# Kernel tuning notes

Hardware: AMD Instinct MI355X
Metric: run time of the kernel (lower is better)

## Reference

```python
import jax, jax.numpy as jnp
import numpy as np

N_EMBD = 512
N_HEAD = 8
HEAD = N_EMBD // N_HEAD
EPS = 1e-5

def layernorm(x, g, b):
    mu = jnp.mean(x, axis=-1, keepdims=True)
    var = jnp.mean(jnp.square(x - mu), axis=-1, keepdims=True)
    return (x - mu) * jax.lax.rsqrt(var + EPS) * g + b

def setup_inputs() -> dict:
    key = jax.random.key(0)
    ks = jax.random.split(key, 12)
    B, T, C, H, D = 32, 512, N_EMBD, N_HEAD, HEAD
    s = lambda fan: 1.0 / np.sqrt(fan)
    return {
        "x": jax.random.normal(ks[0], (B, T, C), jnp.float32),
        "wq": jax.random.normal(ks[1], (H, C, D), jnp.float32) * s(C),
        "wk": jax.random.normal(ks[2], (H, C, D), jnp.float32) * s(C),
        "wv": jax.random.normal(ks[3], (H, C, D), jnp.float32) * s(C),
        "w_proj": jax.random.normal(ks[4], (C, C), jnp.float32) * s(C),
        "b_proj": jnp.zeros((C,), jnp.float32),
        "w1": jax.random.normal(ks[5], (C, 4 * C), jnp.float32) * s(C),
        "b1": jnp.zeros((4 * C,), jnp.float32),
        "w2": jax.random.normal(ks[6], (4 * C, C), jnp.float32) * s(4 * C),
        "b2": jnp.zeros((C,), jnp.float32),
        "ln1_g": jnp.ones((C,), jnp.float32),
        "ln1_b": jnp.zeros((C,), jnp.float32),
        "ln2_g": jnp.ones((C,), jnp.float32),
        "ln2_b": jnp.zeros((C,), jnp.float32),
    }

def reference(x, wq, wk, wv, w_proj, b_proj, w1, b1, w2, b2, ln1_g, ln1_b, ln2_g, ln2_b):
    B, T, C = x.shape
    h = layernorm(x, ln1_g, ln1_b)
    q = jnp.einsum('btc,hcd->bhtd', h, wq)
    k = jnp.einsum('btc,hcd->bhtd', h, wk)
    v = jnp.einsum('btc,hcd->bhtd', h, wv)
    # NB: original scales by n_embd**-0.5 (C), not head_size
    scores = jnp.einsum('bhtd,bhsd->bhts', q, k) * (C ** -0.5)
    causal = jnp.tril(jnp.ones((T, T), bool))
    scores = jnp.where(causal, scores, -jnp.inf)
    attn = jax.nn.softmax(scores, axis=-1)
    o = jnp.einsum('bhts,bhsd->bhtd', attn, v)  # [B,H,T,D]
    o = jnp.transpose(o, (0, 2, 1, 3)).reshape(B, T, C)  # concat heads
    x = x + o @ w_proj + b_proj
    h2 = layernorm(x, ln2_g, ln2_b)
    ffn = jax.nn.relu(h2 @ w1 + b1) @ w2 + b2
    return x + ffn
```

## Files before the change

kernel.cpp:

```cpp
#include <hip/hip_runtime.h>
#include <hip/hip_bf16.h>


#define B_  32
#define T_  512
#define C_  512
#define H_  8
#define D_  64
#define BT  (B_*T_)
#define CF  2048

typedef __hip_bfloat16 bf16;
typedef __attribute__((ext_vector_type(8))) short bf16x8;
typedef __attribute__((ext_vector_type(4))) float f32x4;
typedef __attribute__((ext_vector_type(4))) short short4v;

__device__ __forceinline__ float bf2f(bf16 x) { return __bfloat162float(x); }
__device__ __forceinline__ bf16  f2bf(float x){ return __float2bfloat16(x); }
__device__ __forceinline__ short f2bf_bits(float f){
    bf16 h = __float2bfloat16(f);
    return *reinterpret_cast<short*>(&h);
}
__device__ __forceinline__ float bfbits2f(short s){
    unsigned u = ((unsigned)(unsigned short)s) << 16;
    return __uint_as_float(u);
}

#define AS_G __attribute__((address_space(1)))
#define AS_L __attribute__((address_space(3)))

__global__ __launch_bounds__(256) void transpose_all(const float* __restrict__ wq,
                                                     const float* __restrict__ wk,
                                                     const float* __restrict__ wv,
                                                     const float* __restrict__ wproj,
                                                     const float* __restrict__ w1,
                                                     const float* __restrict__ w2,
                                                     bf16* __restrict__ wt)
{
    const int t = blockIdx.x;
    const float* src; int K, Nn, k0, n0; size_t dstoff;
    if (t < 192) {
        const int which = t / 64, w = t % 64, hh = w >> 3, kt = w & 7;
        src = (which == 0 ? wq : which == 1 ? wk : wv) + (size_t)hh * 512 * 64;
        K = 512; Nn = 64; k0 = kt * 64; n0 = 0;
        dstoff = (size_t)(which * 512 + hh * 64) * 512;
    } else if (t < 256) {
        const int i = t - 192;
        src = wproj; K = 512; Nn = 512; n0 = (i & 7) * 64; k0 = (i >> 3) * 64;
        dstoff = (size_t)1536 * 512;
    } else if (t < 512) {
        const int i = t - 256;
        src = w1; K = 512; Nn = 2048; n0 = (i & 31) * 64; k0 = (i >> 5) * 64;
        dstoff = (size_t)2048 * 512;
    } else {
        const int i = t - 512;
        src = w2; K = 2048; Nn = 512; n0 = (i & 7) * 64; k0 = (i >> 3) * 64;
        dstoff = (size_t)2048 * 512 + (size_t)2048 * 512;
    }

    __shared__ float tl[64][65];
    const int tid = threadIdx.x;
    #pragma unroll
    for (int j = 0; j < 16; ++j) {
        const int e = j * 256 + tid, r = e >> 6, c = e & 63;
        tl[r][c] = src[(size_t)(k0 + r) * Nn + n0 + c];
    }
    __syncthreads();
    #pragma unroll
    for (int j = 0; j < 16; ++j) {
        const int e = j * 256 + tid, n = e >> 6, kk = e & 63;
        wt[dstoff + (size_t)(n0 + n) * K + k0 + kk] = f2bf(tl[kk][n]);
    }
}

__global__ __launch_bounds__(256) void ln_kernel(const float* __restrict__ x,
                                                 const float* __restrict__ g,
                                                 const float* __restrict__ b,
                                                 bf16* __restrict__ out)
{
    const int row = blockIdx.x;
    const int tid = threadIdx.x;
    const float* xr = x + (size_t)row * C_;
    float v0 = xr[tid], v1 = xr[tid + 256];

    __shared__ float red[4];

    float s = v0 + v1;
    #pragma unroll
    for (int off = 32; off > 0; off >>= 1) s += __shfl_down(s, off, 64);
    if ((tid & 63) == 0) red[tid >> 6] = s;
    __syncthreads();
    const float mean = (red[0] + red[1] + red[2] + red[3]) * (1.0f / C_);
    __syncthreads();

    float d0 = v0 - mean, d1 = v1 - mean;
    float vs = d0 * d0 + d1 * d1;
    #pragma unroll
    for (int off = 32; off > 0; off >>= 1) vs += __shfl_down(vs, off, 64);
    if ((tid & 63) == 0) red[tid >> 6] = vs;
    __syncthreads();
    const float var  = (red[0] + red[1] + red[2] + red[3]) * (1.0f / C_);
    const float rstd = rsqrtf(var + 1e-5f);

    bf16* orow = out + (size_t)row * C_;
    orow[tid]       = f2bf(d0 * rstd * g[tid]       + b[tid]);
    orow[tid + 256] = f2bf(d1 * rstd * g[tid + 256] + b[tid + 256]);
}

template<bool QKV, bool RELU, bool OUT_BF16>
__global__ __launch_bounds__(256, 2) void mfma_gemm(const bf16* __restrict__ A,
                                                    const bf16* __restrict__ Bt,
                                                    const float* __restrict__ bias,
                                                    const float* __restrict__ res,
                                                    void* __restrict__ outp,
                                                    int N, int K)
{
    __shared__ __align__(16) bf16 As[2][128 * 64];
    __shared__ __align__(16) bf16 Bs[2][128 * 64];

    const int tid  = threadIdx.x;
    const int wave = tid >> 6, lane = tid & 63;
    const int l16  = lane & 15, quad = lane >> 4;
    const int wm   = wave >> 1, wn = wave & 1;

    const int nwg = gridDim.x * gridDim.y;
    int bid = blockIdx.y * gridDim.x + blockIdx.x;
    bid = (bid & 7) * (nwg >> 3) + (bid >> 3);
    const int tn = (bid % gridDim.x) * 128;
    const int tm = (bid / gridDim.x) * 128;
    const bool vblk = QKV && (tn >= 1024);

    f32x4 acc[4][4];
    #pragma unroll
    for (int i = 0; i < 4; ++i)
        #pragma unroll
        for (int j = 0; j < 4; ++j) acc[i][j] = (f32x4){0.f, 0.f, 0.f, 0.f};

    auto STAGE = [&](int buf, int k0) {
        #pragma unroll
        for (int j = 0; j < 4; ++j) {
            const int g = j * 256 + tid;
            const int row = g >> 3, phys = g & 7;
            const int c = phys ^ (row & 7);
            __builtin_amdgcn_global_load_lds((const AS_G void*)(A  + (size_t)(tm + row) * K + k0 + c * 8),
                                             (AS_L void*)&As[buf][(size_t)g * 8], 16, 0, 0);
            __builtin_amdgcn_global_load_lds((const AS_G void*)(Bt + (size_t)(tn + row) * K + k0 + c * 8),
                                             (AS_L void*)&Bs[buf][(size_t)g * 8], 16, 0, 0);
        }
    };

    STAGE(0, 0);
    __syncthreads();

    int cur = 0;
    for (int k0 = 0; k0 < K; k0 += 64) {
        if (k0 + 64 < K) STAGE(cur ^ 1, k0 + 64);

        #pragma unroll
        for (int half = 0; half < 2; ++half) {
            bf16x8 af[4], bfr[4];
            #pragma unroll
            for (int mf = 0; mf < 4; ++mf) {
                const int r = wm * 64 + mf * 16 + l16;
                const int p = (half * 4 + quad) ^ (r & 7);
                af[mf] = *(const bf16x8*)&As[cur][r * 64 + p * 8];
            }
            #pragma unroll
            for (int nf = 0; nf < 4; ++nf) {
                const int r = wn * 64 + nf * 16 + l16;
                const int p = (half * 4 + quad) ^ (r & 7);
                bfr[nf] = *(const bf16x8*)&Bs[cur][r * 64 + p * 8];
            }
            if (vblk) {
                #pragma unroll
                for (int mf = 0; mf < 4; ++mf)
                    #pragma unroll
                    for (int nf = 0; nf < 4; ++nf)
                        acc[mf][nf] = __builtin_amdgcn_mfma_f32_16x16x32_bf16(af[mf], bfr[nf], acc[mf][nf], 0, 0, 0);
            } else {
                #pragma unroll
                for (int mf = 0; mf < 4; ++mf)
                    #pragma unroll
                    for (int nf = 0; nf < 4; ++nf)
                        acc[mf][nf] = __builtin_amdgcn_mfma_f32_16x16x32_bf16(bfr[nf], af[mf], acc[mf][nf], 0, 0, 0);
            }
        }

        __syncthreads();
        cur ^= 1;
    }

    if (QKV) {
        bf16* qkv = (bf16*)outp;
        if (!vblk) {
            const int which = tn >> 9;
            bf16* dst = qkv + (size_t)which * (8u << 20);
            #pragma unroll
            for (int mf = 0; mf < 4; ++mf) {
                const int m = tm + wm * 64 + mf * 16 + l16;
                const int bb = m >> 9, t = m & 511;
                #pragma unroll
                for (int nf = 0; nf < 4; ++nf) {
                    const int nb = tn + wn * 64 + nf * 16 + quad * 4;
                    const int hh = (nb >> 6) & 7, dd = nb & 63;
                    short4v pk;
                    #pragma unroll
                    for (int r = 0; r < 4; ++r) pk[r] = f2bf_bits(acc[mf][nf][r]);
                    *(short4v*)&dst[((size_t)(bb * 8 + hh) * 512 + t) * 64 + dd] = pk;
                }
            }
        } else {
            bf16* dst = qkv + (size_t)2 * (8u << 20);
            #pragma unroll
            for (int mf = 0; mf < 4; ++mf) {
                const int mb = tm + wm * 64 + mf * 16 + quad * 4;
                const int bb = mb >> 9, t = mb & 511;
                #pragma unroll
                for (int nf = 0; nf < 4; ++nf) {
                    const int n = tn + wn * 64 + nf * 16 + l16;
                    const int hh = (n >> 6) & 7, dd = n & 63;
                    short4v pk;
                    #pragma unroll
                    for (int r = 0; r < 4; ++r) pk[r] = f2bf_bits(acc[mf][nf][r]);
                    *(short4v*)&dst[((size_t)(bb * 8 + hh) * 64 + dd) * 512 + t] = pk;
                }
            }
        }
    } else {
        #pragma unroll
        for (int mf = 0; mf < 4; ++mf) {
            const int m = tm + wm * 64 + mf * 16 + l16;
            #pragma unroll
            for (int nf = 0; nf < 4; ++nf) {
                const int nb = tn + wn * 64 + nf * 16 + quad * 4;
                f32x4 a = acc[mf][nf];
                if (bias) a += *(const f32x4*)&bias[nb];
                if (RELU) {
                    #pragma unroll
                    for (int r = 0; r < 4; ++r) a[r] = fmaxf(a[r], 0.0f);
                }
                if (res)  a += *(const f32x4*)&res[(size_t)m * N + nb];
                if (OUT_BF16) {
                    short4v pk;
                    #pragma unroll
                    for (int r = 0; r < 4; ++r) pk[r] = f2bf_bits(a[r]);
                    *(short4v*)&((bf16*)outp)[(size_t)m * N + nb] = pk;
                } else {
                    *(f32x4*)&((float*)outp)[(size_t)m * N + nb] = a;
                }
            }
        }
    }
}

__global__ __launch_bounds__(256) void attn_kernel(const bf16* __restrict__ q,
                                                   const bf16* __restrict__ kM,
                                                   const bf16* __restrict__ vT,
                                                   bf16* __restrict__ o)
{
    __shared__ __align__(16) bf16 Ks[64][72];
    __shared__ __align__(16) bf16 Vt[64][72];
    __shared__ __align__(16) bf16 Pw[4][16][72];

    const int qt   = gridDim.x - 1 - blockIdx.x;
    const int bh   = blockIdx.y;
    const int tid  = threadIdx.x;
    const int wave = tid >> 6, lane = tid & 63;
    const int l16  = lane & 15, quad = lane >> 4;
    const int qw   = qt * 64 + wave * 16;

    const float scale = 0.04419417382415922f;
    bf16x8 qa[2];
    #pragma unroll
    for (int c = 0; c < 2; ++c) {
        const bf16* qp = q + ((size_t)bh * T_ + qw + l16) * 64 + c * 32 + quad * 8;
        bf16x8 t = *(const bf16x8*)qp;
        #pragma unroll
        for (int j = 0; j < 8; ++j) t[j] = f2bf_bits(bfbits2f(t[j]) * scale);
        qa[c] = t;
    }

    float m_i[4], l_i[4];
    f32x4 Of[4];
    #pragma unroll
    for (int r = 0; r < 4; ++r) { m_i[r] = -1e30f; l_i[r] = 0.0f; }
    #pragma unroll
    for (int f = 0; f < 4; ++f) Of[f] = (f32x4){0.f, 0.f, 0.f, 0.f};

    for (int kt = 0; kt <= qt; ++kt) {
        const int k0 = kt * 64;
        __syncthreads();
        #pragma unroll
        for (int c2 = 0; c2 < 2; ++c2) {
            const int ch = tid + c2 * 256;
            const int row = ch >> 3, e8 = (ch & 7) * 8;
            *(uint4*)&Ks[row][e8] = *(const uint4*)(kM + ((size_t)bh * T_ + k0 + row) * 64 + e8);
            *(uint4*)&Vt[row][e8] = *(const uint4*)(vT + ((size_t)bh * 64 + row) * T_ + k0 + e8);
        }
        __syncthreads();

        f32x4 Sf[4];
        #pragma unroll
        for (int kf = 0; kf < 4; ++kf) {
            bf16x8 b0 = *(const bf16x8*)&Ks[kf * 16 + l16][quad * 8];
            bf16x8 b1 = *(const bf16x8*)&Ks[kf * 16 + l16][32 + quad * 8];
            f32x4 z = (f32x4){0.f, 0.f, 0.f, 0.f};
            z = __builtin_amdgcn_mfma_f32_16x16x32_bf16(qa[0], b0, z, 0, 0, 0);
            z = __builtin_amdgcn_mfma_f32_16x16x32_bf16(qa[1], b1, z, 0, 0, 0);
            Sf[kf] = z;
        }

        if (kt == qt) {
            #pragma unroll
            for (int kf = 0; kf < 4; ++kf)
                #pragma unroll
                for (int r = 0; r < 4; ++r)
                    if (k0 + kf * 16 + l16 > qw + quad * 4 + r) Sf[kf][r] = -1e30f;
        }

        float mnew[4], alpha[4];
        #pragma unroll
        for (int r = 0; r < 4; ++r) {
            float v = fmaxf(fmaxf(Sf[0][r], Sf[1][r]), fmaxf(Sf[2][r], Sf[3][r]));
            v = fmaxf(v, __shfl_xor(v, 1, 64));
            v = fmaxf(v, __shfl_xor(v, 2, 64));
            v = fmaxf(v, __shfl_xor(v, 4, 64));
            v = fmaxf(v, __shfl_xor(v, 8, 64));
            mnew[r]  = fmaxf(m_i[r], v);
            alpha[r] = __expf(m_i[r] - mnew[r]);
            m_i[r]   = mnew[r];
        }

        float rs[4] = {0.f, 0.f, 0.f, 0.f};
        #pragma unroll
        for (int kf = 0; kf < 4; ++kf) {
            #pragma unroll
            for (int r = 0; r < 4; ++r) {
                float p = __expf(Sf[kf][r] - mnew[r]);
                rs[r] += p;
                Pw[wave][quad * 4 + r][kf * 16 + l16] = f2bf(p);
            }
        }
        #pragma unroll
        for (int r = 0; r < 4; ++r) {
            rs[r] += __shfl_xor(rs[r], 1, 64);
            rs[r] += __shfl_xor(rs[r], 2, 64);
            rs[r] += __shfl_xor(rs[r], 4, 64);
            rs[r] += __shfl_xor(rs[r], 8, 64);
            l_i[r] = l_i[r] * alpha[r] + rs[r];
        }
        #pragma unroll
        for (int f = 0; f < 4; ++f)
            #pragma unroll
            for (int r = 0; r < 4; ++r)
                Of[f][r] *= alpha[r];

        bf16x8 pa0 = *(const bf16x8*)&Pw[wave][l16][quad * 8];
        bf16x8 pa1 = *(const bf16x8*)&Pw[wave][l16][32 + quad * 8];
        #pragma unroll
        for (int f = 0; f < 4; ++f) {
            bf16x8 vb0 = *(const bf16x8*)&Vt[f * 16 + l16][quad * 8];
            bf16x8 vb1 = *(const bf16x8*)&Vt[f * 16 + l16][32 + quad * 8];
            Of[f] = __builtin_amdgcn_mfma_f32_16x16x32_bf16(pa0, vb0, Of[f], 0, 0, 0);
            Of[f] = __builtin_amdgcn_mfma_f32_16x16x32_bf16(pa1, vb1, Of[f], 0, 0, 0);
        }
    }

    const int b = bh >> 3, hh = bh & 7;
    #pragma unroll
    for (int r = 0; r < 4; ++r) {
        const float inv = 1.0f / l_i[r];
        const int t = qw + quad * 4 + r;
        #pragma unroll
        for (int f = 0; f < 4; ++f)
            o[((size_t)b * T_ + t) * C_ + hh * 64 + f * 16 + l16] = f2bf(Of[f][r] * inv);
    }
}

extern "C" void kernel_launch(void* const* d_in, const int* in_sizes, int n_in,
                              void* d_out, int out_size, void* d_ws, size_t ws_size,
                              hipStream_t stream)
{
    const float* x     = (const float*)d_in[0];
    const float* wq    = (const float*)d_in[1];
    const float* wk    = (const float*)d_in[2];
    const float* wv    = (const float*)d_in[3];
    const float* wproj = (const float*)d_in[4];
    const float* bproj = (const float*)d_in[5];
    const float* w1    = (const float*)d_in[6];
    const float* b1    = (const float*)d_in[7];
    const float* w2    = (const float*)d_in[8];
    const float* b2    = (const float*)d_in[9];
    const float* ln1g  = (const float*)d_in[10];
    const float* ln1b  = (const float*)d_in[11];
    const float* ln2g  = (const float*)d_in[12];
    const float* ln2b  = (const float*)d_in[13];

    char* ws = (char*)d_ws;
    bf16*  h    = (bf16*)(ws + 0);
    bf16*  q    = (bf16*)(ws + ((size_t)16 << 20));
    bf16*  k    = (bf16*)(ws + ((size_t)32 << 20));
    bf16*  v    = (bf16*)(ws + ((size_t)48 << 20));
    bf16*  mid  = (bf16*)(ws + 0);
    bf16*  o    = (bf16*)(ws + ((size_t)64 << 20));
    bf16*  h2   = (bf16*)(ws + ((size_t)80 << 20));
    bf16*  wt   = (bf16*)(ws + ((size_t)96 << 20));
    bf16*  projt = wt + (size_t)1536 * 512;
    bf16*  w1t   = wt + (size_t)2048 * 512;
    bf16*  w2t   = wt + (size_t)4096 * 512;
    float* x1    = (float*)d_out;

    transpose_all<<<768, 256, 0, stream>>>(wq, wk, wv, wproj, w1, w2, wt);

    ln_kernel<<<BT, 256, 0, stream>>>(x, ln1g, ln1b, h);

    mfma_gemm<true,  false, true ><<<dim3(12, 128), 256, 0, stream>>>(h, wt, nullptr, nullptr, q, 1536, 512);

    attn_kernel<<<dim3(8, B_ * H_), 256, 0, stream>>>(q, k, v, o);

    mfma_gemm<false, false, false><<<dim3(4, 128), 256, 0, stream>>>(o, projt, bproj, x, x1, 512, 512);

    ln_kernel<<<BT, 256, 0, stream>>>(x1, ln2g, ln2b, h2);

    mfma_gemm<false, true,  true ><<<dim3(16, 128), 256, 0, stream>>>(h2, w1t, b1, nullptr, mid, 2048, 512);

    mfma_gemm<false, false, false><<<dim3(4, 128), 256, 0, stream>>>(mid, w2t, b2, x1, (float*)d_out, 512, 2048);
}
```

Measured before the change: 356.6 us.

## Pair causal query tiles per block with double-buffered async K/V staging

Each attention workgroup now handles two query tiles (qt and 7-qt), so every block does the same amount of causal work and shares each staged K/V tile between both. K/V tiles go through global_load_lds into swizzled double buffers, so the next tile loads while the current one is computed, and one barrier per iteration replaces two. Block IDs are remapped for locality, launch bounds request 2 blocks per SM, and the grid is halved. The cost is higher register pressure from two sets of accumulators, and the code depends on AS_G/AS_L macros that are defined elsewhere in the file.

```diff
diff --git a/kernel.cpp b/kernel.cpp
--- a/kernel.cpp
+++ b/kernel.cpp
@@ -253,127 +253,158 @@
     }
 }
 
-__global__ __launch_bounds__(256) void attn_kernel(const bf16* __restrict__ q,
-                                                   const bf16* __restrict__ kM,
-                                                   const bf16* __restrict__ vT,
-                                                   bf16* __restrict__ o)
+
+#define ATTN_TILE(qa, m_i, l_i, Of, qw, qtT)                                          \
+  do {                                                                                \
+    f32x4 Sf[4];                                                                      \
+    _Pragma("unroll")                                                                 \
+    for (int kf = 0; kf < 4; ++kf) {                                                  \
+        const int row = kf * 16 + l16;                                                \
+        bf16x8 b0 = *(const bf16x8*)&Ks[cur][row * 64 + ((quad ^ (row & 7)) * 8)];    \
+        bf16x8 b1 = *(const bf16x8*)&Ks[cur][row * 64 + (((4 + quad) ^ (row & 7)) * 8)]; \
+        f32x4 z = (f32x4){0.f, 0.f, 0.f, 0.f};                                        \
+        z = __builtin_amdgcn_mfma_f32_16x16x32_bf16(qa[0], b0, z, 0, 0, 0);           \
+        z = __builtin_amdgcn_mfma_f32_16x16x32_bf16(qa[1], b1, z, 0, 0, 0);           \
+        Sf[kf] = z;                                                                   \
+    }                                                                                 \
+    if (kt == qtT) {                                                                  \
+        _Pragma("unroll")                                                             \
+        for (int kf = 0; kf < 4; ++kf)                                                \
+            _Pragma("unroll")                                                         \
+            for (int r = 0; r < 4; ++r)                                               \
+                if (kt * 64 + kf * 16 + l16 > (qw) + quad * 4 + r) Sf[kf][r] = -1e30f;\
+    }                                                                                 \
+    float mnew[4], alpha[4];                                                          \
+    _Pragma("unroll")                                                                 \
+    for (int r = 0; r < 4; ++r) {                                                     \
+        float v = fmaxf(fmaxf(Sf[0][r], Sf[1][r]), fmaxf(Sf[2][r], Sf[3][r]));        \
+        v = fmaxf(v, __shfl_xor(v, 1, 64));                                           \
+        v = fmaxf(v, __shfl_xor(v, 2, 64));                                           \
+        v = fmaxf(v, __shfl_xor(v, 4, 64));                                           \
+        v = fmaxf(v, __shfl_xor(v, 8, 64));                                           \
+        mnew[r]   = fmaxf(m_i[r], v);                                                 \
+        alpha[r]  = __expf(m_i[r] - mnew[r]);                                         \
+        m_i[r]    = mnew[r];                                                          \
+    }                                                                                 \
+    float rs[4] = {0.f, 0.f, 0.f, 0.f};                                               \
+    _Pragma("unroll")                                                                 \
+    for (int kf = 0; kf < 4; ++kf) {                                                  \
+        _Pragma("unroll")                                                             \
+        for (int r = 0; r < 4; ++r) {                                                 \
+            float p = __expf(Sf[kf][r] - mnew[r]);                                    \
+            rs[r] += p;                                                               \
+            Pw[wave][quad * 4 + r][kf * 16 + l16] = f2bf(p);                          \
+        }                                                                             \
+    }                                                                                 \
+    _Pragma("unroll")                                                                 \
+    for (int r = 0; r < 4; ++r) {                                                     \
+        rs[r] += __shfl_xor(rs[r], 1, 64);                                            \
+        rs[r] += __shfl_xor(rs[r], 2, 64);                                            \
+        rs[r] += __shfl_xor(rs[r], 4, 64);                                            \
+        rs[r] += __shfl_xor(rs[r], 8, 64);                                            \
+        l_i[r] = l_i[r] * alpha[r] + rs[r];                                           \
+    }                                                                                 \
+    _Pragma("unroll")                                                                 \
+    for (int f = 0; f < 4; ++f)                                                       \
+        _Pragma("unroll")                                                             \
+        for (int r = 0; r < 4; ++r)                                                   \
+            Of[f][r] *= alpha[r];                                                     \
+    bf16x8 pa0 = *(const bf16x8*)&Pw[wave][l16][quad * 8];                            \
+    bf16x8 pa1 = *(const bf16x8*)&Pw[wave][l16][32 + quad * 8];                       \
+    _Pragma("unroll")                                                                 \
+    for (int f = 0; f < 4; ++f) {                                                     \
+        const int vrow = f * 16 + l16;                                                \
+        bf16x8 vb0 = *(const bf16x8*)&Vt[cur][vrow * 64 + ((quad ^ (vrow & 7)) * 8)]; \
+        bf16x8 vb1 = *(const bf16x8*)&Vt[cur][vrow * 64 + (((4 + quad) ^ (vrow & 7)) * 8)]; \
+        Of[f] = __builtin_amdgcn_mfma_f32_16x16x32_bf16(pa0, vb0, Of[f], 0, 0, 0);    \
+        Of[f] = __builtin_amdgcn_mfma_f32_16x16x32_bf16(pa1, vb1, Of[f], 0, 0, 0);    \
+    }                                                                                 \
+  } while (0)
+
+__global__ __launch_bounds__(256, 2) void attn_kernel(const bf16* __restrict__ q,
+                                                      const bf16* __restrict__ kM,
+                                                      const bf16* __restrict__ vT,
+                                                      bf16* __restrict__ o)
 {
-    __shared__ __align__(16) bf16 Ks[64][72];
-    __shared__ __align__(16) bf16 Vt[64][72];
+    __shared__ __align__(16) bf16 Ks[2][64 * 64];
+    __shared__ __align__(16) bf16 Vt[2][64 * 64];
     __shared__ __align__(16) bf16 Pw[4][16][72];
 
-    const int qt   = gridDim.x - 1 - blockIdx.x;
-    const int bh   = blockIdx.y;
     const int tid  = threadIdx.x;
     const int wave = tid >> 6, lane = tid & 63;
     const int l16  = lane & 15, quad = lane >> 4;
-    const int qw   = qt * 64 + wave * 16;
+
+    const int nwg = gridDim.x * gridDim.y;
+    int bid = blockIdx.y * gridDim.x + blockIdx.x;
+    bid = (bid & 7) * (nwg >> 3) + (bid >> 3);
+    const int pair = bid & 3;
+    const int bh   = bid >> 2;
+
+    const int qt0 = pair, qt1 = 7 - pair;
+    const int qw0 = qt0 * 64 + wave * 16;
+    const int qw1 = qt1 * 64 + wave * 16;
 
     const float scale = 0.04419417382415922f;
-    bf16x8 qa[2];
+    bf16x8 qa0[2], qa1[2];
     #pragma unroll
     for (int c = 0; c < 2; ++c) {
-        const bf16* qp = q + ((size_t)bh * T_ + qw + l16) * 64 + c * 32 + quad * 8;
-        bf16x8 t = *(const bf16x8*)qp;
-        #pragma unroll
-        for (int j = 0; j < 8; ++j) t[j] = f2bf_bits(bfbits2f(t[j]) * scale);
-        qa[c] = t;
-    }
-
-    float m_i[4], l_i[4];
-    f32x4 Of[4];
-    #pragma unroll
-    for (int r = 0; r < 4; ++r) { m_i[r] = -1e30f; l_i[r] = 0.0f; }
-    #pragma unroll
-    for (int f = 0; f < 4; ++f) Of[f] = (f32x4){0.f, 0.f, 0.f, 0.f};
-
-    for (int kt = 0; kt <= qt; ++kt) {
+        bf16x8 t0 = *(const bf16x8*)(q + ((size_t)bh * T_ + qw0 + l16) * 64 + c * 32 + quad * 8);
+        bf16x8 t1 = *(const bf16x8*)(q + ((size_t)bh * T_ + qw1 + l16) * 64 + c * 32 + quad * 8);
+        #pragma unroll
+        for (int j = 0; j < 8; ++j) {
+            t0[j] = f2bf_bits(bfbits2f(t0[j]) * scale);
+            t1[j] = f2bf_bits(bfbits2f(t1[j]) * scale);
+        }
+        qa0[c] = t0; qa1[c] = t1;
+    }
+
+    float m0[4], l0[4], m1[4], l1[4];
+    f32x4 O0[4], O1[4];
+    #pragma unroll
+    for (int r = 0; r < 4; ++r) { m0[r] = -1e30f; l0[r] = 0.f; m1[r] = -1e30f; l1[r] = 0.f; }
+    #pragma unroll
+    for (int f = 0; f < 4; ++f) { O0[f] = (f32x4){0.f,0.f,0.f,0.f}; O1[f] = (f32x4){0.f,0.f,0.f,0.f}; }
+
+    auto STAGE = [&](int buf, int kt) {
         const int k0 = kt * 64;
+        #pragma unroll
+        for (int j = 0; j < 2; ++j) {
+            const int g = j * 256 + tid;
+            const int row = g >> 3, phys = g & 7;
+            const int c = phys ^ (row & 7);
+            __builtin_amdgcn_global_load_lds((const AS_G void*)(kM + ((size_t)bh * T_ + k0 + row) * 64 + c * 8),
+                                             (AS_L void*)&Ks[buf][(size_t)g * 8], 16, 0, 0);
+            __builtin_amdgcn_global_load_lds((const AS_G void*)(vT + ((size_t)bh * 64 + row) * T_ + k0 + c * 8),
+                                             (AS_L void*)&Vt[buf][(size_t)g * 8], 16, 0, 0);
+        }
+    };
+
+    STAGE(0, 0);
+    __syncthreads();
+
+    int cur = 0;
+    for (int kt = 0; kt <= qt1; ++kt) {
+        if (kt < qt1) STAGE(cur ^ 1, kt + 1);
+
+        if (kt <= qt0) ATTN_TILE(qa0, m0, l0, O0, qw0, qt0);
+        ATTN_TILE(qa1, m1, l1, O1, qw1, qt1);
+
         __syncthreads();
-        #pragma unroll
-        for (int c2 = 0; c2 < 2; ++c2) {
-            const int ch = tid + c2 * 256;
-            const int row = ch >> 3, e8 = (ch & 7) * 8;
-            *(uint4*)&Ks[row][e8] = *(const uint4*)(kM + ((size_t)bh * T_ + k0 + row) * 64 + e8);
-            *(uint4*)&Vt[row][e8] = *(const uint4*)(vT + ((size_t)bh * 64 + row) * T_ + k0 + e8);
-        }
-        __syncthreads();
-
-        f32x4 Sf[4];
-        #pragma unroll
-        for (int kf = 0; kf < 4; ++kf) {
-            bf16x8 b0 = *(const bf16x8*)&Ks[kf * 16 + l16][quad * 8];
-            bf16x8 b1 = *(const bf16x8*)&Ks[kf * 16 + l16][32 + quad * 8];
-            f32x4 z = (f32x4){0.f, 0.f, 0.f, 0.f};
-            z = __builtin_amdgcn_mfma_f32_16x16x32_bf16(qa[0], b0, z, 0, 0, 0);
-            z = __builtin_amdgcn_mfma_f32_16x16x32_bf16(qa[1], b1, z, 0, 0, 0);
-            Sf[kf] = z;
-        }
-
-        if (kt == qt) {
-            #pragma unroll
-            for (int kf = 0; kf < 4; ++kf)
-                #pragma unroll
-                for (int r = 0; r < 4; ++r)
-                    if (k0 + kf * 16 + l16 > qw + quad * 4 + r) Sf[kf][r] = -1e30f;
-        }
-
-        float mnew[4], alpha[4];
-        #pragma unroll
-        for (int r = 0; r < 4; ++r) {
-            float v = fmaxf(fmaxf(Sf[0][r], Sf[1][r]), fmaxf(Sf[2][r], Sf[3][r]));
-            v = fmaxf(v, __shfl_xor(v, 1, 64));
-            v = fmaxf(v, __shfl_xor(v, 2, 64));
-            v = fmaxf(v, __shfl_xor(v, 4, 64));
-            v = fmaxf(v, __shfl_xor(v, 8, 64));
-            mnew[r]  = fmaxf(m_i[r], v);
-            alpha[r] = __expf(m_i[r] - mnew[r]);
-            m_i[r]   = mnew[r];
-        }
-
-        float rs[4] = {0.f, 0.f, 0.f, 0.f};
-        #pragma unroll
-        for (int kf = 0; kf < 4; ++kf) {
-            #pragma unroll
-            for (int r = 0; r < 4; ++r) {
-                float p = __expf(Sf[kf][r] - mnew[r]);
-                rs[r] += p;
-                Pw[wave][quad * 4 + r][kf * 16 + l16] = f2bf(p);
-            }
-        }
-        #pragma unroll
-        for (int r = 0; r < 4; ++r) {
-            rs[r] += __shfl_xor(rs[r], 1, 64);
-            rs[r] += __shfl_xor(rs[r], 2, 64);
-            rs[r] += __shfl_xor(rs[r], 4, 64);
-            rs[r] += __shfl_xor(rs[r], 8, 64);
-            l_i[r] = l_i[r] * alpha[r] + rs[r];
-        }
-        #pragma unroll
-        for (int f = 0; f < 4; ++f)
-            #pragma unroll
-            for (int r = 0; r < 4; ++r)
-                Of[f][r] *= alpha[r];
-
-        bf16x8 pa0 = *(const bf16x8*)&Pw[wave][l16][quad * 8];
-        bf16x8 pa1 = *(const bf16x8*)&Pw[wave][l16][32 + quad * 8];
+        cur ^= 1;
+    }
+
+    const int b = bh >> 3, hh = bh & 7;
+    #pragma unroll
+    for (int r = 0; r < 4; ++r) {
+        const float inv0 = 1.0f / l0[r];
+        const float inv1 = 1.0f / l1[r];
+        const int t0 = qw0 + quad * 4 + r;
+        const int t1 = qw1 + quad * 4 + r;
         #pragma unroll
         for (int f = 0; f < 4; ++f) {
-            bf16x8 vb0 = *(const bf16x8*)&Vt[f * 16 + l16][quad * 8];
-            bf16x8 vb1 = *(const bf16x8*)&Vt[f * 16 + l16][32 + quad * 8];
-            Of[f] = __builtin_amdgcn_mfma_f32_16x16x32_bf16(pa0, vb0, Of[f], 0, 0, 0);
-            Of[f] = __builtin_amdgcn_mfma_f32_16x16x32_bf16(pa1, vb1, Of[f], 0, 0, 0);
-        }
-    }
-
-    const int b = bh >> 3, hh = bh & 7;
-    #pragma unroll
-    for (int r = 0; r < 4; ++r) {
-        const float inv = 1.0f / l_i[r];
-        const int t = qw + quad * 4 + r;
-        #pragma unroll
-        for (int f = 0; f < 4; ++f)
-            o[((size_t)b * T_ + t) * C_ + hh * 64 + f * 16 + l16] = f2bf(Of[f][r] * inv);
+            o[((size_t)b * T_ + t0) * C_ + hh * 64 + f * 16 + l16] = f2bf(O0[f][r] * inv0);
+            o[((size_t)b * T_ + t1) * C_ + hh * 64 + f * 16 + l16] = f2bf(O1[f][r] * inv1);
+        }
     }
 }
 
@@ -416,7 +447,7 @@
 
     mfma_gemm<true,  false, true ><<<dim3(12, 128), 256, 0, stream>>>(h, wt, nullptr, nullptr, q, 1536, 512);
 
-    attn_kernel<<<dim3(8, B_ * H_), 256, 0, stream>>>(q, k, v, o);
+    attn_kernel<<<dim3(4, B_ * H_), 256, 0, stream>>>(q, k, v, o);
 
     mfma_gemm<false, false, false><<<dim3(4, 128), 256, 0, stream>>>(o, projt, bproj, x, x1, 512, 512);
 
```

After: 335.6 us. 5.9% less time.
